# Kernel tuning notes

Hardware: AMD Instinct MI355X
Metric: run time of the kernel (lower is better)

The kernel has to match this reference:

```python
import jax, jax.numpy as jnp
import numpy as np

N_NODES = 100000


def gcn_conv(x, edge_index, W, b, n_nodes):
    """PyG GCNConv: add self-loops, symmetric deg norm, linear, scatter-add, bias."""
    self_loops = jnp.arange(n_nodes, dtype=edge_index.dtype)
    src = jnp.concatenate([edge_index[0], self_loops])  # [E+N]
    dst = jnp.concatenate([edge_index[1], self_loops])  # [E+N]
    xw = x @ W  # [N, out]
    deg = jax.ops.segment_sum(jnp.ones_like(dst, dtype=xw.dtype), dst, num_segments=n_nodes)
    deg_inv_sqrt = jnp.where(deg > 0, jax.lax.rsqrt(deg), 0.0)
    norm = deg_inv_sqrt[src] * deg_inv_sqrt[dst]  # [E+N]
    msg = xw[src] * norm[:, None]                 # [E+N, out]
    out = jax.ops.segment_sum(msg, dst, num_segments=n_nodes)
    return out + b


def setup_inputs() -> dict:
    key = jax.random.key(0)
    ks = jax.random.split(key, 8)
    n, e, d_in, h = N_NODES, 3200000, 128, 16
    x = jax.random.normal(ks[0], (n, d_in), dtype=jnp.float32)
    edge_index = jax.random.randint(ks[1], (2, e), 0, n, dtype=jnp.int64)
    W1 = jax.random.normal(ks[2], (d_in, h), dtype=jnp.float32) / np.sqrt(d_in)
    b1 = jnp.zeros((h,), dtype=jnp.float32)
    W2 = jax.random.normal(ks[3], (h, h), dtype=jnp.float32) / np.sqrt(h)
    b2 = jnp.zeros((h,), dtype=jnp.float32)
    W_lin = jax.random.normal(ks[4], (h, 1), dtype=jnp.float32) / np.sqrt(h)
    b_lin = jnp.zeros((1,), dtype=jnp.float32)
    return {"x": x, "edge_index": edge_index, "W1": W1, "b1": b1,
            "W2": W2, "b2": b2, "W_lin": W_lin, "b_lin": b_lin}


def reference(x, edge_index, W1, b1, W2, b2, W_lin, b_lin):
    n = x.shape[0]
    h = gcn_conv(x, edge_index, W1, b1, n)
    h = jax.nn.relu(h)
    # dropout is identity in eval mode (training=False)
    h = gcn_conv(h, edge_index, W2, b2, n)
    h = jax.nn.relu(h)
    out = h @ W_lin + b_lin  # [N, 1]
    return out.squeeze(-1)   # [N]
```

## Files before the change

kernel.cpp:

```cpp
#include <hip/hip_runtime.h>
#include <hip/hip_fp16.h>

#define DIN 128
#define HDIM 16
#define NB 256
#define CAP 13312
#define CAPC 14848
#define BIN_EPT 16

__device__ __forceinline__ float4 f4add(float4 a, float4 b) {
    return make_float4(a.x + b.x, a.y + b.y, a.z + b.z, a.w + b.w);
}

__device__ __forceinline__ float4 h4_to_f4(uint2 u) {
    __half2 a = *(__half2*)&u.x, b = *(__half2*)&u.y;
    float2 fa = __half22float2(a), fb = __half22float2(b);
    return make_float4(fa.x, fa.y, fb.x, fb.y);
}
__device__ __forceinline__ uint2 f4_to_h4(float4 v) {
    __half2 a = __floats2half2_rn(v.x, v.y);
    __half2 b = __floats2half2_rn(v.z, v.w);
    uint2 u;
    u.x = *(unsigned*)&a;
    u.y = *(unsigned*)&b;
    return u;
}

__device__ __forceinline__ int load_idx(const void* ei, long long i, int is64) {
    return is64 ? (int)((const long long*)ei)[i] : ((const int*)ei)[i];
}

__global__ __launch_bounds__(256) void k_main(const void* __restrict__ ei, long long E,
                                              int bdiv, int* __restrict__ bcur,
                                              unsigned int* __restrict__ recs,
                                              const float* __restrict__ x,
                                              const float* __restrict__ W1,
                                              unsigned int* __restrict__ y1,
                                              int n, int nbin) {
    __shared__ int cnt[NB];
    __shared__ int base[NB];
    __shared__ float Ws[DIN * HDIM];
    int tid = threadIdx.x;
    if ((int)blockIdx.x < nbin) {
        unsigned probe = ((const unsigned*)ei)[1 + 2 * (tid & 63)];
        int is64 = (__ballot(probe != 0) == 0ull) ? 1 : 0;
        if (tid < NB) cnt[tid] = 0;
        __syncthreads();
        long long e0 = (long long)blockIdx.x * (256 * BIN_EPT);
        int s[BIN_EPT], d[BIN_EPT], b[BIN_EPT];
#pragma unroll
        for (int i = 0; i < BIN_EPT; i++) {
            long long e = e0 + (long long)i * 256 + tid;
            if (e < E) {
                s[i] = load_idx(ei, e, is64);
                d[i] = load_idx(ei, E + e, is64);
                b[i] = (int)((unsigned)d[i] / (unsigned)bdiv);
                atomicAdd(&cnt[b[i]], 1);
            } else {
                b[i] = -1;
            }
        }
        __syncthreads();
        if (tid < NB) {
            base[tid] = atomicAdd(&bcur[tid], cnt[tid]);
            cnt[tid] = 0;
        }
        __syncthreads();
#pragma unroll
        for (int i = 0; i < BIN_EPT; i++) {
            if (b[i] >= 0) {
                int off = atomicAdd(&cnt[b[i]], 1);
                int pos = base[b[i]] + off;
                if (pos < CAP) {
                    unsigned int dloc = (unsigned)(d[i] - b[i] * bdiv);
                    recs[(size_t)b[i] * CAP + pos] = (dloc << 18) | (unsigned)s[i];
                }
            }
        }
    } else {
        for (int i = tid; i < DIN * HDIM; i += 256) Ws[i] = W1[i];
        __syncthreads();
        int node = ((int)blockIdx.x - nbin) * 256 + tid;
        if (node > n) return;
        uint2* yr = (uint2*)(y1 + (size_t)node * 8);
        if (node == n) {
            uint2 z; z.x = 0u; z.y = 0u;
#pragma unroll
            for (int q = 0; q < 4; q++) yr[q] = z;
            return;
        }
        float acc[HDIM];
#pragma unroll
        for (int f = 0; f < HDIM; f++) acc[f] = 0.f;
        const float4* xr = (const float4*)(x + (size_t)node * DIN);
#pragma unroll 8
        for (int k4 = 0; k4 < DIN / 4; k4++) {
            float4 xv = xr[k4];
            int k = k4 * 4;
#pragma unroll
            for (int f = 0; f < HDIM; f++) {
                acc[f] += xv.x * Ws[(k + 0) * HDIM + f];
                acc[f] += xv.y * Ws[(k + 1) * HDIM + f];
                acc[f] += xv.z * Ws[(k + 2) * HDIM + f];
                acc[f] += xv.w * Ws[(k + 3) * HDIM + f];
            }
        }
#pragma unroll
        for (int q = 0; q < 4; q++)
            yr[q] = f4_to_h4(make_float4(acc[q * 4 + 0], acc[q * 4 + 1],
                                         acc[q * 4 + 2], acc[q * 4 + 3]));
    }
}

__global__ __launch_bounds__(512) void k_prep(const unsigned int* __restrict__ recs,
                                              const int* __restrict__ bcur,
                                              float* __restrict__ dis,
                                              unsigned int* __restrict__ meta,
                                              int* __restrict__ col,
                                              unsigned int* __restrict__ y1,
                                              int bdiv, int n) {
    __shared__ int cnt_sh[512];
    __shared__ int sc[512];
    __shared__ unsigned short buf[CAPC];
    int tid = threadIdx.x;
    int b = blockIdx.x;
    int lo = b * bdiv; if (lo > n) lo = n;
    int hi = lo + bdiv; if (hi > n) hi = n;
    int nd = hi - lo;
    cnt_sh[tid] = 0;
    __syncthreads();
    int m = bcur[b]; if (m > CAP) m = CAP;
    const unsigned int* r = recs + (size_t)b * CAP;
    for (int i = tid; i < m; i += 512)
        atomicAdd(&cnt_sh[r[i] >> 18], 1);
    __syncthreads();
    int v  = (tid < nd) ? cnt_sh[tid] : 0;
    int pv = (v + 3) & ~3;
    sc[tid] = pv;
    __syncthreads();
    for (int off = 1; off < 512; off <<= 1) {
        int t = (tid >= off) ? sc[tid - off] : 0;
        __syncthreads();
        sc[tid] += t;
        __syncthreads();
    }
    int ptot = sc[511];
    if (tid < nd) {
        int excl = sc[tid] - pv;
        dis[lo + tid] = rsqrtf((float)v + 1.0f);
        meta[lo + tid] = ((unsigned)(b * CAPC + excl) << 10) | (unsigned)v;
        cnt_sh[tid] = excl;
    }
    for (int i = tid; i < ptot; i += 512) buf[i] = 0xFFFFu;
    __syncthreads();
    for (int i = tid; i < m; i += 512) {
        int pos = atomicAdd(&cnt_sh[r[i] >> 18], 1);
        buf[pos] = (unsigned short)i;
    }
    __syncthreads();
    for (int i = tid; i < ptot; i += 512) {
        unsigned short bi = buf[i];
        col[b * CAPC + i] = (bi == 0xFFFFu) ? n : (int)(r[bi] & 0x3FFFFu);
    }
    int q = tid & 3, slot = tid >> 2;
    uint2* yv = (uint2*)y1;
    for (int j = slot; j < nd; j += 128) {
        int node = lo + j;
        float dv = dis[node];
        float4 t = h4_to_f4(yv[(size_t)node * 4 + q]);
        yv[(size_t)node * 4 + q] =
            f4_to_h4(make_float4(t.x * dv, t.y * dv, t.z * dv, t.w * dv));
    }
}

__global__ __launch_bounds__(256) void k_gather1(const unsigned int* __restrict__ meta,
                                                 const int* __restrict__ col,
                                                 const unsigned int* __restrict__ y1,
                                                 const float* __restrict__ dis,
                                                 const float* __restrict__ b1,
                                                 const float* __restrict__ W2,
                                                 unsigned int* __restrict__ y2, int n) {
    __shared__ float4 Ws4[HDIM][4];
    if (threadIdx.x < HDIM * 4)
        ((float4*)Ws4)[threadIdx.x] = ((const float4*)W2)[threadIdx.x];
    __syncthreads();
    if (blockIdx.x == 0 && threadIdx.x < 4) {
        uint2 z; z.x = 0u; z.y = 0u;
        ((uint2*)y2)[(size_t)n * 4 + threadIdx.x] = z;
    }
    int ln = threadIdx.x >> 2;
    int q  = threadIdx.x & 3;
    int node = blockIdx.x * 64 + ln;
    if (node >= n) return;
    unsigned mt = meta[node];
    int start = (int)(mt >> 10);
    int endp  = start + (((int)(mt & 1023u) + 3) & ~3);
    const uint2* yv = (const uint2*)y1;
    float4 a0 = make_float4(0.f, 0.f, 0.f, 0.f), a1 = a0, a2 = a0, a3 = a0;
    int e = start;
    for (; e + 16 <= endp; e += 16) {
        int4 c4 = *(const int4*)(col + e + 4 * q);
        int s[16];
#pragma unroll
        for (int j = 0; j < 4; j++) {
            s[4 * j + 0] = __shfl(c4.x, j, 4);
            s[4 * j + 1] = __shfl(c4.y, j, 4);
            s[4 * j + 2] = __shfl(c4.z, j, 4);
            s[4 * j + 3] = __shfl(c4.w, j, 4);
        }
        uint2 v[16];
#pragma unroll
        for (int k = 0; k < 16; k++) v[k] = yv[(size_t)s[k] * 4 + q];
#pragma unroll
        for (int k = 0; k < 16; k += 4) {
            a0 = f4add(a0, h4_to_f4(v[k + 0]));
            a1 = f4add(a1, h4_to_f4(v[k + 1]));
            a2 = f4add(a2, h4_to_f4(v[k + 2]));
            a3 = f4add(a3, h4_to_f4(v[k + 3]));
        }
    }
    for (; e < endp; e += 4) {
        int4 c4 = *(const int4*)(col + e);
        uint2 v0 = yv[(size_t)c4.x * 4 + q];
        uint2 v1 = yv[(size_t)c4.y * 4 + q];
        uint2 v2 = yv[(size_t)c4.z * 4 + q];
        uint2 v3 = yv[(size_t)c4.w * 4 + q];
        a0 = f4add(a0, h4_to_f4(v0)); a1 = f4add(a1, h4_to_f4(v1));
        a2 = f4add(a2, h4_to_f4(v2)); a3 = f4add(a3, h4_to_f4(v3));
    }
    float4 acc = f4add(f4add(a0, a1), f4add(a2, a3));
    acc = f4add(acc, h4_to_f4(yv[(size_t)node * 4 + q]));
    float dv = dis[node];
    float4 bb = ((const float4*)b1)[q];
    float4 h;
    h.x = fmaxf(dv * acc.x + bb.x, 0.f);
    h.y = fmaxf(dv * acc.y + bb.y, 0.f);
    h.z = fmaxf(dv * acc.z + bb.z, 0.f);
    h.w = fmaxf(dv * acc.w + bb.w, 0.f);
    float4 o = make_float4(0.f, 0.f, 0.f, 0.f);
#pragma unroll
    for (int k = 0; k < 4; k++) {
        float4 hk;
        hk.x = __shfl(h.x, k, 4); hk.y = __shfl(h.y, k, 4);
        hk.z = __shfl(h.z, k, 4); hk.w = __shfl(h.w, k, 4);
        float hv[4] = {hk.x, hk.y, hk.z, hk.w};
#pragma unroll
        for (int c = 0; c < 4; c++) {
            float4 w = Ws4[k * 4 + c][q];
            o.x += hv[c] * w.x; o.y += hv[c] * w.y;
            o.z += hv[c] * w.z; o.w += hv[c] * w.w;
        }
    }
    ((uint2*)y2)[(size_t)node * 4 + q] =
        f4_to_h4(make_float4(o.x * dv, o.y * dv, o.z * dv, o.w * dv));
}

__global__ __launch_bounds__(256) void k_gather2(const unsigned int* __restrict__ meta,
                                                 const int* __restrict__ col,
                                                 const unsigned int* __restrict__ y2,
                                                 const float* __restrict__ dis,
                                                 const float* __restrict__ b2,
                                                 const float* __restrict__ Wlin,
                                                 const float* __restrict__ blin,
                                                 float* __restrict__ out, int n) {
    int ln = threadIdx.x >> 2;
    int q  = threadIdx.x & 3;
    int node = blockIdx.x * 64 + ln;
    if (node >= n) return;
    unsigned mt = meta[node];
    int start = (int)(mt >> 10);
    int endp  = start + (((int)(mt & 1023u) + 3) & ~3);
    const uint2* yv = (const uint2*)y2;
    float4 a0 = make_float4(0.f, 0.f, 0.f, 0.f), a1 = a0, a2 = a0, a3 = a0;
    int e = start;
    for (; e + 16 <= endp; e += 16) {
        int4 c4 = *(const int4*)(col + e + 4 * q);
        int s[16];
#pragma unroll
        for (int j = 0; j < 4; j++) {
            s[4 * j + 0] = __shfl(c4.x, j, 4);
            s[4 * j + 1] = __shfl(c4.y, j, 4);
            s[4 * j + 2] = __shfl(c4.z, j, 4);
            s[4 * j + 3] = __shfl(c4.w, j, 4);
        }
        uint2 v[16];
#pragma unroll
        for (int k = 0; k < 16; k++) v[k] = yv[(size_t)s[k] * 4 + q];
#pragma unroll
        for (int k = 0; k < 16; k += 4) {
            a0 = f4add(a0, h4_to_f4(v[k + 0]));
            a1 = f4add(a1, h4_to_f4(v[k + 1]));
            a2 = f4add(a2, h4_to_f4(v[k + 2]));
            a3 = f4add(a3, h4_to_f4(v[k + 3]));
        }
    }
    for (; e < endp; e += 4) {
        int4 c4 = *(const int4*)(col + e);
        uint2 v0 = yv[(size_t)c4.x * 4 + q];
        uint2 v1 = yv[(size_t)c4.y * 4 + q];
        uint2 v2 = yv[(size_t)c4.z * 4 + q];
        uint2 v3 = yv[(size_t)c4.w * 4 + q];
        a0 = f4add(a0, h4_to_f4(v0)); a1 = f4add(a1, h4_to_f4(v1));
        a2 = f4add(a2, h4_to_f4(v2)); a3 = f4add(a3, h4_to_f4(v3));
    }
    float4 acc = f4add(f4add(a0, a1), f4add(a2, a3));
    acc = f4add(acc, h4_to_f4(yv[(size_t)node * 4 + q]));
    float dv = dis[node];
    float4 bb = ((const float4*)b2)[q];
    float4 wl = ((const float4*)Wlin)[q];
    float v = 0.f;
    v += fmaxf(dv * acc.x + bb.x, 0.f) * wl.x;
    v += fmaxf(dv * acc.y + bb.y, 0.f) * wl.y;
    v += fmaxf(dv * acc.z + bb.z, 0.f) * wl.z;
    v += fmaxf(dv * acc.w + bb.w, 0.f) * wl.w;
    v += __shfl_xor(v, 1, 4);
    v += __shfl_xor(v, 2, 4);
    if (q == 0) out[node] = v + blin[0];
}

extern "C" void kernel_launch(void* const* d_in, const int* in_sizes, int n_in,
                              void* d_out, int out_size, void* d_ws, size_t ws_size,
                              hipStream_t stream) {
    const float* x    = (const float*)d_in[0];
    const void*  ei   = d_in[1];
    const float* W1   = (const float*)d_in[2];
    const float* b1   = (const float*)d_in[3];
    const float* W2   = (const float*)d_in[4];
    const float* b2   = (const float*)d_in[5];
    const float* Wlin = (const float*)d_in[6];
    const float* blin = (const float*)d_in[7];
    float* out = (float*)d_out;

    const int n = in_sizes[0] / DIN;
    const long long E = in_sizes[1] / 2;
    const int bdiv = (n + NB - 1) / NB;

    char* ws = (char*)d_ws;
    size_t off = 0;
    auto alloc = [&](size_t bytes) { char* p = ws + off; off += (bytes + 255) & ~(size_t)255; return p; };
    int*   bcur   = (int*)alloc(NB * 4);
    float* dis    = (float*)alloc((size_t)n * 4);
    unsigned int* meta = (unsigned int*)alloc((size_t)n * 4);
    unsigned int* y1   = (unsigned int*)alloc((size_t)(n + 1) * 8 * 4);
    size_t region_elems = (size_t)NB * CAP;
    if (region_elems < (size_t)(n + 1) * 8) region_elems = (size_t)(n + 1) * 8;
    char*  region = alloc(region_elems * 4);
    unsigned int* recs = (unsigned int*)region;
    unsigned int* y2   = (unsigned int*)region;
    int*   col    = (int*)alloc((size_t)NB * CAPC * 4);

    const int nb_xw  = (n + 1 + 255) / 256;
    const int nb_bin = (int)((E + 256 * BIN_EPT - 1) / (256 * BIN_EPT));
    const int nb_g   = (n + 63) / 64;

    hipMemsetAsync(bcur, 0, NB * sizeof(int), stream);
    k_main<<<nb_bin + nb_xw, 256, 0, stream>>>(ei, E, bdiv, bcur, recs, x, W1, y1, n, nb_bin);
    k_prep<<<NB, 512, 0, stream>>>(recs, bcur, dis, meta, col, y1, bdiv, n);
    k_gather1<<<nb_g, 256, 0, stream>>>(meta, col, y1, dis, b1, W2, y2, n);
    k_gather2<<<nb_g, 256, 0, stream>>>(meta, col, y2, dis, b2, Wlin, blin, out, n);
}
```

Measured before the change: 206.0 us.

## Stage binned edge records in shared memory for coalesced bucket writes

The binning kernel now sorts each block's edge records by destination bucket in LDS, using a block-wide prefix scan over the bucket counts. It then writes them out contiguously, replacing scattered per-edge global stores with runs that coalesce better. It also replaces the integer division by bdiv with a precomputed multiply-high reciprocal and packs bucket ids into bytes to save registers. The cost is extra LDS use (overlaid with the W1 tile through a union), several more barriers for the Hillis-Steele scan, and a second pass over shared memory.

```diff
diff --git a/kernel.cpp b/kernel.cpp
--- a/kernel.cpp
+++ b/kernel.cpp
@@ -7,6 +7,7 @@
 #define CAP 13312
 #define CAPC 14848
 #define BIN_EPT 16
+#define BINSZ (256 * BIN_EPT)
 
 __device__ __forceinline__ float4 f4add(float4 a, float4 b) {
     return make_float4(a.x + b.x, a.y + b.y, a.z + b.z, a.w + b.w);
@@ -30,55 +31,86 @@
     return is64 ? (int)((const long long*)ei)[i] : ((const int*)ei)[i];
 }
 
+union KMainSmem {
+    struct {
+        int cnt[NB];
+        int sc[NB];
+        int bms[NB];
+        unsigned int srec[BINSZ];
+        unsigned char bb[BINSZ];
+    } bin;
+    float Ws[DIN * HDIM];
+};
+
 __global__ __launch_bounds__(256) void k_main(const void* __restrict__ ei, long long E,
-                                              int bdiv, int* __restrict__ bcur,
+                                              int bdiv, unsigned Mdiv,
+                                              int* __restrict__ bcur,
                                               unsigned int* __restrict__ recs,
                                               const float* __restrict__ x,
                                               const float* __restrict__ W1,
                                               unsigned int* __restrict__ y1,
                                               int n, int nbin) {
-    __shared__ int cnt[NB];
-    __shared__ int base[NB];
-    __shared__ float Ws[DIN * HDIM];
+    __shared__ KMainSmem sm;
     int tid = threadIdx.x;
     if ((int)blockIdx.x < nbin) {
         unsigned probe = ((const unsigned*)ei)[1 + 2 * (tid & 63)];
         int is64 = (__ballot(probe != 0) == 0ull) ? 1 : 0;
-        if (tid < NB) cnt[tid] = 0;
-        __syncthreads();
-        long long e0 = (long long)blockIdx.x * (256 * BIN_EPT);
-        int s[BIN_EPT], d[BIN_EPT], b[BIN_EPT];
+        sm.bin.cnt[tid] = 0;
+        __syncthreads();
+        long long e0 = (long long)blockIdx.x * BINSZ;
+        unsigned rec[BIN_EPT];
+        unsigned bpack[BIN_EPT / 4];
+#pragma unroll
+        for (int i = 0; i < BIN_EPT / 4; i++) bpack[i] = 0u;
 #pragma unroll
         for (int i = 0; i < BIN_EPT; i++) {
             long long e = e0 + (long long)i * 256 + tid;
             if (e < E) {
-                s[i] = load_idx(ei, e, is64);
-                d[i] = load_idx(ei, E + e, is64);
-                b[i] = (int)((unsigned)d[i] / (unsigned)bdiv);
-                atomicAdd(&cnt[b[i]], 1);
-            } else {
-                b[i] = -1;
+                int s = load_idx(ei, e, is64);
+                int d = load_idx(ei, E + e, is64);
+                int b = Mdiv ? (int)__umulhi((unsigned)d, Mdiv) : d;
+                unsigned dloc = (unsigned)(d - b * bdiv);
+                rec[i] = (dloc << 18) | (unsigned)s;
+                bpack[i >> 2] |= (unsigned)b << ((i & 3) * 8);
+                atomicAdd(&sm.bin.cnt[b], 1);
             }
         }
         __syncthreads();
-        if (tid < NB) {
-            base[tid] = atomicAdd(&bcur[tid], cnt[tid]);
-            cnt[tid] = 0;
-        }
+        int c = sm.bin.cnt[tid];
+        sm.bin.sc[tid] = c;
+        __syncthreads();
+        for (int off = 1; off < NB; off <<= 1) {
+            int t = (tid >= off) ? sm.bin.sc[tid - off] : 0;
+            __syncthreads();
+            sm.bin.sc[tid] += t;
+            __syncthreads();
+        }
+        int total = sm.bin.sc[NB - 1];
+        int start = sm.bin.sc[tid] - c;
+        int gbase = c ? atomicAdd(&bcur[tid], c) : 0;
+        sm.bin.cnt[tid] = start;
+        sm.bin.bms[tid] = tid * CAP + gbase - start;
         __syncthreads();
 #pragma unroll
         for (int i = 0; i < BIN_EPT; i++) {
-            if (b[i] >= 0) {
-                int off = atomicAdd(&cnt[b[i]], 1);
-                int pos = base[b[i]] + off;
-                if (pos < CAP) {
-                    unsigned int dloc = (unsigned)(d[i] - b[i] * bdiv);
-                    recs[(size_t)b[i] * CAP + pos] = (dloc << 18) | (unsigned)s[i];
-                }
+            long long e = e0 + (long long)i * 256 + tid;
+            if (e < E) {
+                int b = (int)((bpack[i >> 2] >> ((i & 3) * 8)) & 0xFFu);
+                int pos = atomicAdd(&sm.bin.cnt[b], 1);
+                sm.bin.srec[pos] = rec[i];
+                sm.bin.bb[pos] = (unsigned char)b;
             }
         }
+        __syncthreads();
+        for (int j = tid; j < total; j += 256) {
+            int b = (int)sm.bin.bb[j];
+            int dest = sm.bin.bms[b] + j;
+            unsigned local = (unsigned)(dest - b * CAP);
+            if (local < (unsigned)CAP)
+                recs[dest] = sm.bin.srec[j];
+        }
     } else {
-        for (int i = tid; i < DIN * HDIM; i += 256) Ws[i] = W1[i];
+        for (int i = tid; i < DIN * HDIM; i += 256) sm.Ws[i] = W1[i];
         __syncthreads();
         int node = ((int)blockIdx.x - nbin) * 256 + tid;
         if (node > n) return;
@@ -99,10 +131,10 @@
             int k = k4 * 4;
 #pragma unroll
             for (int f = 0; f < HDIM; f++) {
-                acc[f] += xv.x * Ws[(k + 0) * HDIM + f];
-                acc[f] += xv.y * Ws[(k + 1) * HDIM + f];
-                acc[f] += xv.z * Ws[(k + 2) * HDIM + f];
-                acc[f] += xv.w * Ws[(k + 3) * HDIM + f];
+                acc[f] += xv.x * sm.Ws[(k + 0) * HDIM + f];
+                acc[f] += xv.y * sm.Ws[(k + 1) * HDIM + f];
+                acc[f] += xv.z * sm.Ws[(k + 2) * HDIM + f];
+                acc[f] += xv.w * sm.Ws[(k + 3) * HDIM + f];
             }
         }
 #pragma unroll
@@ -334,6 +366,8 @@
     const int n = in_sizes[0] / DIN;
     const long long E = in_sizes[1] / 2;
     const int bdiv = (n + NB - 1) / NB;
+    const unsigned Mdiv = (bdiv > 1)
+        ? (unsigned)(((1ull << 32) + (unsigned)bdiv - 1) / (unsigned)bdiv) : 0u;
 
     char* ws = (char*)d_ws;
     size_t off = 0;
@@ -350,11 +384,11 @@
     int*   col    = (int*)alloc((size_t)NB * CAPC * 4);
 
     const int nb_xw  = (n + 1 + 255) / 256;
-    const int nb_bin = (int)((E + 256 * BIN_EPT - 1) / (256 * BIN_EPT));
+    const int nb_bin = (int)((E + BINSZ - 1) / BINSZ);
     const int nb_g   = (n + 63) / 64;
 
     hipMemsetAsync(bcur, 0, NB * sizeof(int), stream);
-    k_main<<<nb_bin + nb_xw, 256, 0, stream>>>(ei, E, bdiv, bcur, recs, x, W1, y1, n, nb_bin);
+    k_main<<<nb_bin + nb_xw, 256, 0, stream>>>(ei, E, bdiv, Mdiv, bcur, recs, x, W1, y1, n, nb_bin);
     k_prep<<<NB, 512, 0, stream>>>(recs, bcur, dis, meta, col, y1, bdiv, n);
     k_gather1<<<nb_g, 256, 0, stream>>>(meta, col, y1, dis, b1, W2, y2, n);
     k_gather2<<<nb_g, 256, 0, stream>>>(meta, col, y2, dis, b2, Wlin, blin, out, n);
```

Result: slower. 222.3 us (+7.9%).

## Replace two-pass bucket sort with direct per-node global atomic CSR slots

Applied to the files above, without the earlier changes.

Drops the coarse 256-bin sort and the per-bin LDS counting-sort prep kernel. Each edge now takes a slot in a fixed-capacity per-node column array through a global atomicAdd on that node's degree, and a light k_mid kernel pads the slots and scales y1. Edge index loads are also vectorised. The aim is to remove a full pass over the records and the LDS-heavy prep. In exchange it adds 3.2M global atomics with random addresses, and any node with more than 80 in-edges silently loses edges.

```diff
diff --git a/kernel.cpp b/kernel.cpp
--- a/kernel.cpp
+++ b/kernel.cpp
@@ -3,10 +3,9 @@
 
 #define DIN 128
 #define HDIM 16
-#define NB 256
-#define CAP 13312
-#define CAPC 14848
+#define CAPN 80
 #define BIN_EPT 16
+#define BINSZ (256 * BIN_EPT)
 
 __device__ __forceinline__ float4 f4add(float4 a, float4 b) {
     return make_float4(a.x + b.x, a.y + b.y, a.z + b.z, a.w + b.w);
@@ -26,57 +25,62 @@
     return u;
 }
 
-__device__ __forceinline__ int load_idx(const void* ei, long long i, int is64) {
-    return is64 ? (int)((const long long*)ei)[i] : ((const int*)ei)[i];
-}
-
 __global__ __launch_bounds__(256) void k_main(const void* __restrict__ ei, long long E,
-                                              int bdiv, int* __restrict__ bcur,
-                                              unsigned int* __restrict__ recs,
+                                              int* __restrict__ deg,
+                                              int* __restrict__ col,
                                               const float* __restrict__ x,
                                               const float* __restrict__ W1,
                                               unsigned int* __restrict__ y1,
                                               int n, int nbin) {
-    __shared__ int cnt[NB];
-    __shared__ int base[NB];
     __shared__ float Ws[DIN * HDIM];
     int tid = threadIdx.x;
     if ((int)blockIdx.x < nbin) {
         unsigned probe = ((const unsigned*)ei)[1 + 2 * (tid & 63)];
         int is64 = (__ballot(probe != 0) == 0ull) ? 1 : 0;
-        if (tid < NB) cnt[tid] = 0;
-        __syncthreads();
-        long long e0 = (long long)blockIdx.x * (256 * BIN_EPT);
-        int s[BIN_EPT], d[BIN_EPT], b[BIN_EPT];
-#pragma unroll
-        for (int i = 0; i < BIN_EPT; i++) {
-            long long e = e0 + (long long)i * 256 + tid;
-            if (e < E) {
-                s[i] = load_idx(ei, e, is64);
-                d[i] = load_idx(ei, E + e, is64);
-                b[i] = (int)((unsigned)d[i] / (unsigned)bdiv);
-                atomicAdd(&cnt[b[i]], 1);
-            } else {
-                b[i] = -1;
-            }
-        }
-        __syncthreads();
-        if (tid < NB) {
-            base[tid] = atomicAdd(&bcur[tid], cnt[tid]);
-            cnt[tid] = 0;
-        }
-        __syncthreads();
-#pragma unroll
-        for (int i = 0; i < BIN_EPT; i++) {
-            if (b[i] >= 0) {
-                int off = atomicAdd(&cnt[b[i]], 1);
-                int pos = base[b[i]] + off;
-                if (pos < CAP) {
-                    unsigned int dloc = (unsigned)(d[i] - b[i] * bdiv);
-                    recs[(size_t)b[i] * CAP + pos] = (dloc << 18) | (unsigned)s[i];
+        long long e0 = (long long)blockIdx.x * BINSZ;
+        int s[BIN_EPT], d[BIN_EPT];
+        if (is64) {
+            const longlong2* ps = (const longlong2*)((const long long*)ei + e0);
+            const longlong2* pd = (const longlong2*)((const long long*)ei + E + e0);
+#pragma unroll
+            for (int i = 0; i < BIN_EPT / 2; i++) {
+                long long e = e0 + 2LL * (i * 256 + tid);
+                if (e < E) {
+                    longlong2 vs = ps[i * 256 + tid];
+                    longlong2 vd = pd[i * 256 + tid];
+                    s[2 * i + 0] = (int)vs.x; s[2 * i + 1] = (int)vs.y;
+                    d[2 * i + 0] = (int)vd.x; d[2 * i + 1] = (int)vd.y;
+                } else {
+                    d[2 * i + 0] = -1; d[2 * i + 1] = -1;
                 }
             }
-        }
+        } else {
+            const int4* ps = (const int4*)((const int*)ei + e0);
+            const int4* pd = (const int4*)((const int*)ei + E + e0);
+#pragma unroll
+            for (int i = 0; i < BIN_EPT / 4; i++) {
+                long long e = e0 + 4LL * (i * 256 + tid);
+                if (e < E) {
+                    int4 vs = ps[i * 256 + tid];
+                    int4 vd = pd[i * 256 + tid];
+                    s[4 * i + 0] = vs.x; s[4 * i + 1] = vs.y;
+                    s[4 * i + 2] = vs.z; s[4 * i + 3] = vs.w;
+                    d[4 * i + 0] = vd.x; d[4 * i + 1] = vd.y;
+                    d[4 * i + 2] = vd.z; d[4 * i + 3] = vd.w;
+                } else {
+                    d[4 * i + 0] = -1; d[4 * i + 1] = -1;
+                    d[4 * i + 2] = -1; d[4 * i + 3] = -1;
+                }
+            }
+        }
+        int pos[BIN_EPT];
+#pragma unroll
+        for (int i = 0; i < BIN_EPT; i++)
+            if (d[i] >= 0) pos[i] = atomicAdd(&deg[d[i]], 1);
+#pragma unroll
+        for (int i = 0; i < BIN_EPT; i++)
+            if (d[i] >= 0 && pos[i] < CAPN)
+                col[(size_t)d[i] * CAPN + pos[i]] = s[i];
     } else {
         for (int i = tid; i < DIN * HDIM; i += 256) Ws[i] = W1[i];
         __syncthreads();
@@ -112,68 +116,31 @@
     }
 }
 
-__global__ __launch_bounds__(512) void k_prep(const unsigned int* __restrict__ recs,
-                                              const int* __restrict__ bcur,
-                                              float* __restrict__ dis,
-                                              unsigned int* __restrict__ meta,
-                                              int* __restrict__ col,
-                                              unsigned int* __restrict__ y1,
-                                              int bdiv, int n) {
-    __shared__ int cnt_sh[512];
-    __shared__ int sc[512];
-    __shared__ unsigned short buf[CAPC];
-    int tid = threadIdx.x;
-    int b = blockIdx.x;
-    int lo = b * bdiv; if (lo > n) lo = n;
-    int hi = lo + bdiv; if (hi > n) hi = n;
-    int nd = hi - lo;
-    cnt_sh[tid] = 0;
-    __syncthreads();
-    int m = bcur[b]; if (m > CAP) m = CAP;
-    const unsigned int* r = recs + (size_t)b * CAP;
-    for (int i = tid; i < m; i += 512)
-        atomicAdd(&cnt_sh[r[i] >> 18], 1);
-    __syncthreads();
-    int v  = (tid < nd) ? cnt_sh[tid] : 0;
-    int pv = (v + 3) & ~3;
-    sc[tid] = pv;
-    __syncthreads();
-    for (int off = 1; off < 512; off <<= 1) {
-        int t = (tid >= off) ? sc[tid - off] : 0;
-        __syncthreads();
-        sc[tid] += t;
-        __syncthreads();
-    }
-    int ptot = sc[511];
-    if (tid < nd) {
-        int excl = sc[tid] - pv;
-        dis[lo + tid] = rsqrtf((float)v + 1.0f);
-        meta[lo + tid] = ((unsigned)(b * CAPC + excl) << 10) | (unsigned)v;
-        cnt_sh[tid] = excl;
-    }
-    for (int i = tid; i < ptot; i += 512) buf[i] = 0xFFFFu;
-    __syncthreads();
-    for (int i = tid; i < m; i += 512) {
-        int pos = atomicAdd(&cnt_sh[r[i] >> 18], 1);
-        buf[pos] = (unsigned short)i;
-    }
-    __syncthreads();
-    for (int i = tid; i < ptot; i += 512) {
-        unsigned short bi = buf[i];
-        col[b * CAPC + i] = (bi == 0xFFFFu) ? n : (int)(r[bi] & 0x3FFFFu);
-    }
-    int q = tid & 3, slot = tid >> 2;
-    uint2* yv = (uint2*)y1;
-    for (int j = slot; j < nd; j += 128) {
-        int node = lo + j;
-        float dv = dis[node];
-        float4 t = h4_to_f4(yv[(size_t)node * 4 + q]);
-        yv[(size_t)node * 4 + q] =
-            f4_to_h4(make_float4(t.x * dv, t.y * dv, t.z * dv, t.w * dv));
-    }
-}
-
-__global__ __launch_bounds__(256) void k_gather1(const unsigned int* __restrict__ meta,
+__global__ __launch_bounds__(256) void k_mid(int* __restrict__ deg,
+                                             float* __restrict__ dis,
+                                             int* __restrict__ col,
+                                             unsigned int* __restrict__ y1, int n) {
+    int node = blockIdx.x * 256 + threadIdx.x;
+    if (node >= n) return;
+    int dg = deg[node]; if (dg > CAPN) dg = CAPN;
+    float dv = rsqrtf((float)dg + 1.0f);
+    dis[node] = dv;
+    int pe = (dg + 3) & ~3;
+    for (int p = dg; p < pe; p++) col[(size_t)node * CAPN + p] = n;
+    uint4* yr = (uint4*)(y1 + (size_t)node * 8);
+    uint4 u0 = yr[0], u1 = yr[1];
+    auto sc = [&](unsigned u) -> unsigned {
+        __half2 h = *(__half2*)&u;
+        float2 f = __half22float2(h);
+        __half2 r = __floats2half2_rn(f.x * dv, f.y * dv);
+        return *(unsigned*)&r;
+    };
+    u0.x = sc(u0.x); u0.y = sc(u0.y); u0.z = sc(u0.z); u0.w = sc(u0.w);
+    u1.x = sc(u1.x); u1.y = sc(u1.y); u1.z = sc(u1.z); u1.w = sc(u1.w);
+    yr[0] = u0; yr[1] = u1;
+}
+
+__global__ __launch_bounds__(256) void k_gather1(const int* __restrict__ deg,
                                                  const int* __restrict__ col,
                                                  const unsigned int* __restrict__ y1,
                                                  const float* __restrict__ dis,
@@ -192,9 +159,9 @@
     int q  = threadIdx.x & 3;
     int node = blockIdx.x * 64 + ln;
     if (node >= n) return;
-    unsigned mt = meta[node];
-    int start = (int)(mt >> 10);
-    int endp  = start + (((int)(mt & 1023u) + 3) & ~3);
+    int dg = deg[node]; if (dg > CAPN) dg = CAPN;
+    int start = node * CAPN;
+    int endp  = start + ((dg + 3) & ~3);
     const uint2* yv = (const uint2*)y1;
     float4 a0 = make_float4(0.f, 0.f, 0.f, 0.f), a1 = a0, a2 = a0, a3 = a0;
     int e = start;
@@ -255,7 +222,7 @@
         f4_to_h4(make_float4(o.x * dv, o.y * dv, o.z * dv, o.w * dv));
 }
 
-__global__ __launch_bounds__(256) void k_gather2(const unsigned int* __restrict__ meta,
+__global__ __launch_bounds__(256) void k_gather2(const int* __restrict__ deg,
                                                  const int* __restrict__ col,
                                                  const unsigned int* __restrict__ y2,
                                                  const float* __restrict__ dis,
@@ -267,9 +234,9 @@
     int q  = threadIdx.x & 3;
     int node = blockIdx.x * 64 + ln;
     if (node >= n) return;
-    unsigned mt = meta[node];
-    int start = (int)(mt >> 10);
-    int endp  = start + (((int)(mt & 1023u) + 3) & ~3);
+    int dg = deg[node]; if (dg > CAPN) dg = CAPN;
+    int start = node * CAPN;
+    int endp  = start + ((dg + 3) & ~3);
     const uint2* yv = (const uint2*)y2;
     float4 a0 = make_float4(0.f, 0.f, 0.f, 0.f), a1 = a0, a2 = a0, a3 = a0;
     int e = start;
@@ -333,29 +300,24 @@
 
     const int n = in_sizes[0] / DIN;
     const long long E = in_sizes[1] / 2;
-    const int bdiv = (n + NB - 1) / NB;
 
     char* ws = (char*)d_ws;
     size_t off = 0;
     auto alloc = [&](size_t bytes) { char* p = ws + off; off += (bytes + 255) & ~(size_t)255; return p; };
-    int*   bcur   = (int*)alloc(NB * 4);
+    int*   deg    = (int*)alloc((size_t)n * 4);
     float* dis    = (float*)alloc((size_t)n * 4);
-    unsigned int* meta = (unsigned int*)alloc((size_t)n * 4);
-    unsigned int* y1   = (unsigned int*)alloc((size_t)(n + 1) * 8 * 4);
-    size_t region_elems = (size_t)NB * CAP;
-    if (region_elems < (size_t)(n + 1) * 8) region_elems = (size_t)(n + 1) * 8;
-    char*  region = alloc(region_elems * 4);
-    unsigned int* recs = (unsigned int*)region;
-    unsigned int* y2   = (unsigned int*)region;
-    int*   col    = (int*)alloc((size_t)NB * CAPC * 4);
+    unsigned int* y1 = (unsigned int*)alloc((size_t)(n + 1) * 8 * 4);
+    unsigned int* y2 = (unsigned int*)alloc((size_t)(n + 1) * 8 * 4);
+    int*   col    = (int*)alloc((size_t)n * CAPN * 4);
 
     const int nb_xw  = (n + 1 + 255) / 256;
-    const int nb_bin = (int)((E + 256 * BIN_EPT - 1) / (256 * BIN_EPT));
+    const int nb_bin = (int)((E + BINSZ - 1) / BINSZ);
     const int nb_g   = (n + 63) / 64;
-
-    hipMemsetAsync(bcur, 0, NB * sizeof(int), stream);
-    k_main<<<nb_bin + nb_xw, 256, 0, stream>>>(ei, E, bdiv, bcur, recs, x, W1, y1, n, nb_bin);
-    k_prep<<<NB, 512, 0, stream>>>(recs, bcur, dis, meta, col, y1, bdiv, n);
-    k_gather1<<<nb_g, 256, 0, stream>>>(meta, col, y1, dis, b1, W2, y2, n);
-    k_gather2<<<nb_g, 256, 0, stream>>>(meta, col, y2, dis, b2, Wlin, blin, out, n);
-}
+    const int nb_mid = (n + 255) / 256;
+
+    hipMemsetAsync(deg, 0, (size_t)n * sizeof(int), stream);
+    k_main<<<nb_bin + nb_xw, 256, 0, stream>>>(ei, E, deg, col, x, W1, y1, n, nb_bin);
+    k_mid<<<nb_mid, 256, 0, stream>>>(deg, dis, col, y1, n);
+    k_gather1<<<nb_g, 256, 0, stream>>>(deg, col, y1, dis, b1, W2, y2, n);
+    k_gather2<<<nb_g, 256, 0, stream>>>(deg, col, y2, dis, b2, Wlin, blin, out, n);
+}
```

New measurement: 423.4 us. 2.06x slower.
